# Kernel optimization log

Measured on AMD Instinct MI355X. Metric: run time of the kernel, lower is better.

The kernel has to match this reference:

```python
import jax, jax.numpy as jnp
import numpy as np

N = 2048      # num_nodes
B = 64        # batch
D_IN = 2      # input_dim per node
UNITS = 64    # hidden dim
K = 2         # max_diffusion_step
N_SUP = 2     # dual_random_walk -> two supports
M = N_SUP * K + 1           # num_matrices = 5
IN_SIZE = D_IN + UNITS      # 66
E = 65536                   # nnz per support


def setup_inputs() -> dict:
    key = jax.random.key(0)
    ks = jax.random.split(key, 10)
    inputs = jax.random.normal(ks[0], (B, N * D_IN), jnp.float32)
    state = jax.random.normal(ks[1], (B, N * UNITS), jnp.float32)
    edges1 = jax.random.randint(ks[2], (2, E), 0, N)
    vals1 = jax.random.uniform(ks[3], (E,), jnp.float32) / 32.0  # ~row-stochastic scale
    edges2 = jax.random.randint(ks[4], (2, E), 0, N)
    vals2 = jax.random.uniform(ks[5], (E,), jnp.float32) / 32.0
    W_gate = jax.random.normal(ks[6], (IN_SIZE * M, 2 * UNITS), jnp.float32) * 0.08
    b_gate = jnp.ones((2 * UNITS,), jnp.float32)  # bias_start=1.0 for gate
    W_cand = jax.random.normal(ks[7], (IN_SIZE * M, UNITS), jnp.float32) * 0.08
    b_cand = jnp.zeros((UNITS,), jnp.float32)
    return dict(inputs=inputs, state=state, edges1=edges1, vals1=vals1,
                edges2=edges2, vals2=vals2, W_gate=W_gate, b_gate=b_gate,
                W_cand=W_cand, b_cand=b_cand)


def _spmm(rows, cols, vals, x):
    # sparse [N,N] @ dense [N,F] via gather + segment_sum
    return jax.ops.segment_sum(x[cols] * vals[:, None], rows, num_segments=N)


def _dconv(inp, st, supports, W, b, out_dim):
    # inputs/state -> [B, N, F] concat, F = IN_SIZE
    x = jnp.concatenate([inp.reshape(B, N, -1), st.reshape(B, N, -1)], axis=2)
    f = x.shape[2]
    x0 = x.transpose(1, 2, 0).reshape(N, f * B)  # [N, F*B]
    xs = [x0]
    for (rows, cols, vals) in supports:
        x1 = _spmm(rows, cols, vals, x0)
        xs.append(x1)
        xk_1, xk_2 = x1, x0
        for _ in range(2, K + 1):  # Chebyshev recursion: x_k = 2 S x_{k-1} - x_{k-2}
            xk = 2.0 * _spmm(rows, cols, vals, xk_1) - xk_2
            xs.append(xk)
            xk_1, xk_2 = xk, xk_1
    xcat = jnp.stack(xs, 0).reshape(M, N, f, B)
    xcat = xcat.transpose(3, 1, 2, 0).reshape(B * N, f * M)  # [B*N, F*M]
    out = xcat @ W + b
    return out.reshape(B, N * out_dim)


def reference(inputs, state, edges1, vals1, edges2, vals2, W_gate, b_gate, W_cand, b_cand):
    supports = [(edges1[0], edges1[1], vals1), (edges2[0], edges2[1], vals2)]
    value = jax.nn.sigmoid(_dconv(inputs, state, supports, W_gate, b_gate, 2 * UNITS))
    value = value.reshape(B, N, 2 * UNITS)
    r = value[:, :, :UNITS].reshape(B, N * UNITS)
    u = value[:, :, UNITS:].reshape(B, N * UNITS)
    c = jnp.tanh(_dconv(inputs, r * state, supports, W_cand, b_cand, UNITS))
    new_state = u * state + (1.0 - u) * c
    return new_state
```

## Files before the change

### kernel.cpp

```cpp
#include <hip/hip_runtime.h>
#include <stdint.h>

#define NN 2048
#define EE 65536
#define APITCH 360
#define XSN ((size_t)NN*4096)
#define XIN ((size_t)NN*128)

typedef unsigned short u16;
typedef __bf16 bf16x8 __attribute__((ext_vector_type(8)));
typedef float f32x4 __attribute__((ext_vector_type(4)));
typedef float f32x2 __attribute__((ext_vector_type(2)));

__device__ __forceinline__ float bf2f(u16 h){ return __uint_as_float(((unsigned)h)<<16); }
__device__ __forceinline__ u16 f2bf(float f){
  unsigned u = __float_as_uint(f);
  u += 0x7fffu + ((u>>16)&1u);
  return (u16)(u>>16);
}
__device__ __forceinline__ float loadf(const void* p, size_t i, int bfflag){
  return bfflag ? bf2f(((const u16*)p)[i]) : ((const float*)p)[i];
}
__device__ __forceinline__ f32x2 up2(unsigned u){
  f32x2 r; r.x = __uint_as_float(u<<16); r.y = __uint_as_float(u & 0xffff0000u); return r;
}
__device__ __forceinline__ unsigned pk2(f32x2 t){
  return (unsigned)f2bf(t.x) | ((unsigned)f2bf(t.y)<<16);
}
__device__ __forceinline__ void accv(float v, uint4 d, f32x2* a){
  f32x2 vv = {v, v};
  a[0] += vv*up2(d.x); a[1] += vv*up2(d.y);
  a[2] += vv*up2(d.z); a[3] += vv*up2(d.w);
}

__global__ void probe_k(const unsigned* __restrict__ vals, int* __restrict__ flag){
  int i = threadIdx.x;
  unsigned lo = vals[i] & 0xffffu;
  unsigned long long m = __ballot(lo >= 0x2800u && lo < 0x3D80u);
  if (i==0) *flag = (__popcll(m) >= 32) ? 1 : 0;
}

__global__ void hist2_k(const int* __restrict__ e1, const int* __restrict__ e2,
                        int* __restrict__ cnt){
  int b = blockIdx.x;
  if (b < 256) atomicAdd(&cnt[e1[b*256 + threadIdx.x]], 1);
  else atomicAdd(&cnt[2048 + e2[(b-256)*256 + threadIdx.x]], 1);
}

__global__ void scan2_k(const int* __restrict__ cntA, int* __restrict__ rpA, int* __restrict__ curA){
  __shared__ int s[1024];
  const int* cnt = cntA + blockIdx.x*2048;
  int* rp  = rpA  + blockIdx.x*2049;
  int* cur = curA + blockIdx.x*2048;
  int t = threadIdx.x;
  int c0 = cnt[2*t], c1 = cnt[2*t+1];
  int ps = c0 + c1;
  s[t] = ps;
  __syncthreads();
  for (int off=1; off<1024; off<<=1){
    int v = (t>=off) ? s[t-off] : 0;
    __syncthreads();
    s[t] += v;
    __syncthreads();
  }
  int excl = s[t] - ps;
  rp[2*t] = excl;  cur[2*t] = excl;
  rp[2*t+1] = excl + c0;  cur[2*t+1] = excl + c0;
  if (t==0) rp[2048] = EE;
}

__global__ void scatter2_k(const int* __restrict__ e1, const void* __restrict__ v1,
                           const int* __restrict__ e2, const void* __restrict__ v2,
                           int* __restrict__ curA, int2* __restrict__ scvA,
                           const int* __restrict__ flag){
  int bfflag = *flag;
  int b = blockIdx.x;
  const int* rows; const int* cols; const void* vals; int* cur; int2* scv; int e;
  if (b < 256){ rows=e1; cols=e1+EE; vals=v1; cur=curA; scv=scvA; e=b*256+threadIdx.x; }
  else { rows=e2; cols=e2+EE; vals=v2; cur=curA+2048; scv=scvA+EE; e=(b-256)*256+threadIdx.x; }
  int r = rows[e];
  int p = atomicAdd(&cur[r], 1);
  int2 cv; cv.x = cols[e]; cv.y = __float_as_int(loadf(vals, e, bfflag));
  scv[p] = cv;
}

__global__ void pack2_k(const void* __restrict__ Wg, const void* __restrict__ Wc,
                        u16* __restrict__ Wfg, u16* __restrict__ Wfc,
                        const int* __restrict__ flag){
  int bfflag = *flag;
  int b = blockIdx.x;
  const void* W; u16* Wf; int O, OT, i;
  if (b < 176){ W=Wg; Wf=Wfg; O=128; OT=8; i=b*256+threadIdx.x; }
  else { W=Wc; Wf=Wfc; O=64; OT=4; i=(b-176)*256+threadIdx.x; }
  int j = i & 7, L = (i>>3)&63, tq = i>>9;
  int t = tq % OT, q = tq / OT;
  int o = t*16 + (L&15);
  int kk = q*32 + (L>>4)*8 + j;
  float v = 0.f;
  if (kk < 320){ int m = kk>>6, f = (kk&63)+2; v = loadf(W, (size_t)(f*5+m)*O + o, bfflag); }
  else if (kk < 330){ int tt = kk-320; int m = tt>>1, f = tt&1; v = loadf(W, (size_t)(f*5+m)*O + o, bfflag); }
  Wf[i] = f2bf(v);
}

__global__ void build_x0_k(const void* __restrict__ inp, const void* __restrict__ st,
                           u16* __restrict__ XSb, u16* __restrict__ XIb,
                           const int* __restrict__ flag){
  int bfflag = *flag, n = blockIdx.x, tid = threadIdx.x;
  if (bfflag){
    const uint4* sp = (const uint4*)st;
    uint4* xp = (uint4*)(XSb + (size_t)n*4096);
    #pragma unroll
    for (int it=0; it<2; ++it){
      int r = tid + it*256;
      int b = r>>3, v4 = r&7;
      xp[r] = sp[(size_t)b*(NN*8) + (size_t)n*8 + v4];
    }
    if (tid < 64){
      ((unsigned*)XIb)[n*64 + tid] = ((const unsigned*)inp)[(size_t)tid*NN + n];
    }
  } else {
    for (int i=tid; i<4096; i+=256){
      int b=i>>6, f=i&63;
      XSb[(size_t)n*4096+i] = f2bf(((const float*)st)[(size_t)b*(NN*64) + n*64 + f]);
    }
    for (int i=tid; i<128; i+=256){
      int b=i>>1, f=i&1;
      XIb[(size_t)n*128+i] = f2bf(((const float*)inp)[(size_t)b*(NN*2) + n*2 + f]);
    }
  }
}

template<int CHEB>
__global__ __launch_bounds__(64) void spmm_k(
    u16* __restrict__ XSb, u16* __restrict__ XIb,
    const int* __restrict__ rpA, const int2* __restrict__ scvA){
  int sup = blockIdx.y;
  const int* rp = rpA + sup*2049;
  const int2* scv = scvA + sup*EE;
  const int srcm = CHEB ? (sup?3:1) : 0;
  const int dstm = CHEB ? (sup?4:2) : (sup?3:1);
  int tid = threadIdx.x;
  int bx = blockIdx.x;
  if (bx < NN*8){
    int ch = bx & 7, n = bx >> 3;
    int e0 = rp[n], e1 = rp[n+1];
    const uint4* src = (const uint4*)(XSb + srcm*XSN);
    int off = ch*64 + tid;
    f32x2 a[4] = {{0.f,0.f},{0.f,0.f},{0.f,0.f},{0.f,0.f}};
    int e = e0;
    for (; e+3 < e1; e += 4){
      int2 c0=scv[e], c1=scv[e+1], c2=scv[e+2], c3=scv[e+3];
      uint4 d0 = src[((size_t)c0.x<<9) + off];
      uint4 d1 = src[((size_t)c1.x<<9) + off];
      uint4 d2 = src[((size_t)c2.x<<9) + off];
      uint4 d3 = src[((size_t)c3.x<<9) + off];
      accv(__int_as_float(c0.y), d0, a);
      accv(__int_as_float(c1.y), d1, a);
      accv(__int_as_float(c2.y), d2, a);
      accv(__int_as_float(c3.y), d3, a);
    }
    for (; e < e1; ++e){
      int2 c0 = scv[e];
      accv(__int_as_float(c0.y), src[((size_t)c0.x<<9) + off], a);
    }
    uint4* dst = (uint4*)(XSb + dstm*XSN);
    uint4 w;
    if (CHEB){
      uint4 o = ((const uint4*)XSb)[((size_t)n<<9) + off];
      f32x2 t;
      t = 2.f*a[0] - up2(o.x); w.x = pk2(t);
      t = 2.f*a[1] - up2(o.y); w.y = pk2(t);
      t = 2.f*a[2] - up2(o.z); w.z = pk2(t);
      t = 2.f*a[3] - up2(o.w); w.w = pk2(t);
    } else {
      w.x = pk2(a[0]); w.y = pk2(a[1]); w.z = pk2(a[2]); w.w = pk2(a[3]);
    }
    dst[((size_t)n<<9) + off] = w;
  } else {
    int idx = bx - NN*8;
    int n = idx*2 + (tid>>5), m = tid & 31;
    int e0 = rp[n], e1 = rp[n+1];
    const uint2* src = (const uint2*)(XIb + srcm*XIN);
    f32x2 a0 = {0.f,0.f}, a1 = {0.f,0.f};
    for (int e=e0; e<e1; ++e){
      int2 cv = scv[e];
      uint2 d = src[cv.x*32 + m];
      f32x2 vv = {__int_as_float(cv.y), __int_as_float(cv.y)};
      a0 += vv*up2(d.x); a1 += vv*up2(d.y);
    }
    uint2* dst = (uint2*)(XIb + dstm*XIN);
    if (CHEB){
      uint2 o = ((const uint2*)XIb)[n*32 + m];
      a0 = 2.f*a0 - up2(o.x); a1 = 2.f*a1 - up2(o.y);
    }
    uint2 w; w.x = pk2(a0); w.y = pk2(a1);
    dst[n*32 + m] = w;
  }
}

template<int OT, int MODE>
__global__ __launch_bounds__(256) void gemm_k(
    u16* __restrict__ XSb, const u16* __restrict__ XIb,
    const u16* __restrict__ Wf, const void* __restrict__ bias,
    const void* __restrict__ state, void* __restrict__ outp,
    const int* __restrict__ flag){
  __shared__ __align__(16) u16 A[64*APITCH];
  int tid = threadIdx.x, n = blockIdx.x;
  int bfflag = *flag;
  #pragma unroll
  for (int m=0;m<5;m++){
    const uint4* src = (const uint4*)(XSb + (size_t)m*XSN + ((size_t)n<<12));
    #pragma unroll
    for (int it=0; it<2; ++it){
      int r = tid + it*256;
      uint4 d = src[r];
      int b = r>>3, f0 = (r&7)*8;
      *(uint4*)&A[b*APITCH + m*64 + f0] = d;
    }
  }
  for (int i=tid; i<320; i+=256){
    int m = i>>6, b = i&63;
    unsigned v = ((const unsigned*)XIb)[(size_t)m*(XIN/2) + n*64 + b];
    *(unsigned*)&A[b*APITCH + 320 + 2*m] = v;
  }
  for (int i=tid; i<64*15; i+=256){
    int b = i/15, j = i - b*15;
    *(unsigned*)&A[b*APITCH + 330 + 2*j] = 0;
  }
  const int TW = OT/4;
  int lane = tid & 63, w = tid >> 6;
  int m16 = lane & 15, q4 = lane >> 4;
  const bf16x8* wp = (const bf16x8*)Wf;
  bf16x8 wfr[11][TW];
  #pragma unroll
  for (int q=0;q<11;q++){
    #pragma unroll
    for (int i=0;i<TW;i++) wfr[q][i] = wp[(q*OT + (w + 4*i))*64 + lane];
  }
  __syncthreads();
  #pragma unroll
  for (int rt4=0; rt4<4; ++rt4){
    const u16* arow = A + (rt4*16 + m16)*APITCH + q4*8;
    f32x4 acc[TW];
    #pragma unroll
    for (int i=0;i<TW;i++) acc[i] = (f32x4){0.f,0.f,0.f,0.f};
    #pragma unroll
    for (int q=0;q<11;q++){
      bf16x8 af = *((const bf16x8*)(arow + q*32));
      #pragma unroll
      for (int i=0;i<TW;i++)
        acc[i] = __builtin_amdgcn_mfma_f32_16x16x32_bf16(af, wfr[q][i], acc[i], 0, 0, 0);
    }
    #pragma unroll
    for (int i=0;i<TW;i++){
      int t = w + 4*i;
      int o = t*16 + m16;
      float bo = loadf(bias, o, bfflag);
      #pragma unroll
      for (int r=0;r<4;r++){
        int b = rt4*16 + q4*4 + r;
        float x = acc[i][r] + bo;
        if (MODE==0){
          float s = 1.f/(1.f + __expf(-x));
          if (i==0){
            float st = loadf(state, (size_t)b*(NN*64) + (size_t)n*64 + o, bfflag);
            XSb[((size_t)n<<12) + b*64 + o] = f2bf(s*st);
          } else {
            size_t idx = (size_t)b*(NN*64) + (size_t)n*64 + (o-64);
            if (bfflag) ((u16*)outp)[idx] = f2bf(s); else ((float*)outp)[idx] = s;
          }
        } else {
          float c = tanhf(x);
          size_t idx = (size_t)b*(NN*64) + (size_t)n*64 + o;
          float uu = bfflag ? bf2f(((const u16*)outp)[idx]) : ((const float*)outp)[idx];
          float st = loadf(state, idx, bfflag);
          float ns = uu*st + (1.f-uu)*c;
          if (bfflag) ((u16*)outp)[idx] = f2bf(ns); else ((float*)outp)[idx] = ns;
        }
      }
    }
  }
}

extern "C" void kernel_launch(void* const* d_in, const int* in_sizes, int n_in,
                              void* d_out, int out_size, void* d_ws, size_t ws_size,
                              hipStream_t stream) {
  const void* inputs = d_in[0];
  const void* state  = d_in[1];
  const int* edges1 = (const int*)d_in[2];
  const void* vals1  = d_in[3];
  const int* edges2 = (const int*)d_in[4];
  const void* vals2  = d_in[5];
  const void* Wg     = d_in[6];
  const void* bg     = d_in[7];
  const void* Wc     = d_in[8];
  const void* bc     = d_in[9];

  char* ws = (char*)d_ws;
  size_t off = 0;
  auto get = [&](size_t bytes)->void*{
    void* p = ws + off; off = (off + bytes + 255) & ~(size_t)255; return p;
  };
  u16* XSb = (u16*)get(5*XSN*2);
  u16* XIb = (u16*)get(5*XIN*2);
  u16* Wfg = (u16*)get(11*8*64*8*2);
  u16* Wfc = (u16*)get(11*4*64*8*2);
  int* cnt  = (int*)get(2*2048*4);
  int* rp   = (int*)get(2*2049*4);
  int* cur  = (int*)get(2*2048*4);
  int* flag = (int*)get(4);
  int2* scv = (int2*)get((size_t)2*EE*8);

  probe_k<<<1,64,0,stream>>>((const unsigned*)vals1, flag);
  hipMemsetAsync(cnt, 0, 2*2048*4, stream);
  hist2_k<<<512,256,0,stream>>>(edges1, edges2, cnt);
  scan2_k<<<2,1024,0,stream>>>(cnt, rp, cur);
  scatter2_k<<<512,256,0,stream>>>(edges1, vals1, edges2, vals2, cur, scv, flag);
  pack2_k<<<264,256,0,stream>>>(Wg, Wc, Wfg, Wfc, flag);
  build_x0_k<<<NN,256,0,stream>>>(inputs, state, XSb, XIb, flag);

  dim3 sg(NN*8 + NN/2, 2);
  spmm_k<0><<<sg,64,0,stream>>>(XSb, XIb, rp, scv);
  spmm_k<1><<<sg,64,0,stream>>>(XSb, XIb, rp, scv);
  gemm_k<8,0><<<NN,256,0,stream>>>(XSb, XIb, Wfg, bg, state, d_out, flag);
  spmm_k<0><<<sg,64,0,stream>>>(XSb, XIb, rp, scv);
  spmm_k<1><<<sg,64,0,stream>>>(XSb, XIb, rp, scv);
  gemm_k<4,1><<<NN,256,0,stream>>>(XSb, XIb, Wfc, bc, state, d_out, flag);
}
```

Baseline: 447.0 us.

## Widen SpMM per-thread chunk, interleave supports in 1D grid, pre-shift column offsets

The SpMM kernel now has each thread handle 32 bytes (16 bf16 values) per gathered row, using 4 chunks per node instead of 8. Both supports are interleaved in a single 1D grid so the two supports for the same node run in adjacent blocks. Column indices are pre-scaled into byte offsets during CSR scatter so the gather address is a plain add. Outputs use nontemporal stores and the Chebyshev x0 read uses nontemporal loads. This cuts index loads and address math per byte gathered, at the cost of more registers per thread and fewer waves overall.

```diff
diff --git a/kernel.cpp b/kernel.cpp
--- a/kernel.cpp
+++ b/kernel.cpp
@@ -11,6 +11,7 @@
 typedef __bf16 bf16x8 __attribute__((ext_vector_type(8)));
 typedef float f32x4 __attribute__((ext_vector_type(4)));
 typedef float f32x2 __attribute__((ext_vector_type(2)));
+typedef unsigned u32x4 __attribute__((ext_vector_type(4)));
 
 __device__ __forceinline__ float bf2f(u16 h){ return __uint_as_float(((unsigned)h)<<16); }
 __device__ __forceinline__ u16 f2bf(float f){
@@ -27,7 +28,7 @@
 __device__ __forceinline__ unsigned pk2(f32x2 t){
   return (unsigned)f2bf(t.x) | ((unsigned)f2bf(t.y)<<16);
 }
-__device__ __forceinline__ void accv(float v, uint4 d, f32x2* a){
+__device__ __forceinline__ void accv(float v, u32x4 d, f32x2* a){
   f32x2 vv = {v, v};
   a[0] += vv*up2(d.x); a[1] += vv*up2(d.y);
   a[2] += vv*up2(d.z); a[3] += vv*up2(d.w);
@@ -80,7 +81,7 @@
   else { rows=e2; cols=e2+EE; vals=v2; cur=curA+2048; scv=scvA+EE; e=(b-256)*256+threadIdx.x; }
   int r = rows[e];
   int p = atomicAdd(&cur[r], 1);
-  int2 cv; cv.x = cols[e]; cv.y = __float_as_int(loadf(vals, e, bfflag));
+  int2 cv; cv.x = cols[e] << 13; cv.y = __float_as_int(loadf(vals, e, bfflag));
   scv[p] = cv;
 }
 
@@ -134,67 +135,85 @@
 __global__ __launch_bounds__(64) void spmm_k(
     u16* __restrict__ XSb, u16* __restrict__ XIb,
     const int* __restrict__ rpA, const int2* __restrict__ scvA){
-  int sup = blockIdx.y;
-  const int* rp = rpA + sup*2049;
-  const int2* scv = scvA + sup*EE;
-  const int srcm = CHEB ? (sup?3:1) : 0;
-  const int dstm = CHEB ? (sup?4:2) : (sup?3:1);
   int tid = threadIdx.x;
   int bx = blockIdx.x;
   if (bx < NN*8){
-    int ch = bx & 7, n = bx >> 3;
+    int ch = bx & 3, sup = (bx>>2)&1, n = bx >> 3;
+    const int* rp = rpA + sup*2049;
+    const int2* scv = scvA + sup*EE;
+    const int srcm = CHEB ? (sup?3:1) : 0;
+    const int dstm = CHEB ? (sup?4:2) : (sup?3:1);
     int e0 = rp[n], e1 = rp[n+1];
-    const uint4* src = (const uint4*)(XSb + srcm*XSN);
-    int off = ch*64 + tid;
-    f32x2 a[4] = {{0.f,0.f},{0.f,0.f},{0.f,0.f},{0.f,0.f}};
+    unsigned offB = (unsigned)ch*2048 + (unsigned)tid*32;
+    const char* srcp = (const char*)(XSb + (size_t)srcm*XSN) + offB;
+    f32x2 a[8] = {{0.f,0.f},{0.f,0.f},{0.f,0.f},{0.f,0.f},
+                  {0.f,0.f},{0.f,0.f},{0.f,0.f},{0.f,0.f}};
     int e = e0;
-    for (; e+3 < e1; e += 4){
-      int2 c0=scv[e], c1=scv[e+1], c2=scv[e+2], c3=scv[e+3];
-      uint4 d0 = src[((size_t)c0.x<<9) + off];
-      uint4 d1 = src[((size_t)c1.x<<9) + off];
-      uint4 d2 = src[((size_t)c2.x<<9) + off];
-      uint4 d3 = src[((size_t)c3.x<<9) + off];
-      accv(__int_as_float(c0.y), d0, a);
-      accv(__int_as_float(c1.y), d1, a);
-      accv(__int_as_float(c2.y), d2, a);
-      accv(__int_as_float(c3.y), d3, a);
-    }
-    for (; e < e1; ++e){
+    for (; e+1 < e1; e += 2){
+      int2 c0 = scv[e], c1 = scv[e+1];
+      const char* p0 = srcp + (unsigned)c0.x;
+      const char* p1 = srcp + (unsigned)c1.x;
+      u32x4 d00 = *(const u32x4*)p0;
+      u32x4 d01 = *(const u32x4*)(p0+16);
+      u32x4 d10 = *(const u32x4*)p1;
+      u32x4 d11 = *(const u32x4*)(p1+16);
+      float v0 = __int_as_float(c0.y), v1 = __int_as_float(c1.y);
+      accv(v0, d00, a); accv(v0, d01, a+4);
+      accv(v1, d10, a); accv(v1, d11, a+4);
+    }
+    if (e < e1){
       int2 c0 = scv[e];
-      accv(__int_as_float(c0.y), src[((size_t)c0.x<<9) + off], a);
-    }
-    uint4* dst = (uint4*)(XSb + dstm*XSN);
-    uint4 w;
+      const char* p0 = srcp + (unsigned)c0.x;
+      u32x4 d00 = *(const u32x4*)p0;
+      u32x4 d01 = *(const u32x4*)(p0+16);
+      float v0 = __int_as_float(c0.y);
+      accv(v0, d00, a); accv(v0, d01, a+4);
+    }
+    unsigned doff = ((unsigned)n << 13) + offB;
+    char* dstp = (char*)(XSb + (size_t)dstm*XSN) + doff;
+    u32x4 w0, w1;
     if (CHEB){
-      uint4 o = ((const uint4*)XSb)[((size_t)n<<9) + off];
+      u32x4 o0 = __builtin_nontemporal_load((const u32x4*)((const char*)XSb + doff));
+      u32x4 o1 = __builtin_nontemporal_load((const u32x4*)((const char*)XSb + doff + 16));
       f32x2 t;
-      t = 2.f*a[0] - up2(o.x); w.x = pk2(t);
-      t = 2.f*a[1] - up2(o.y); w.y = pk2(t);
-      t = 2.f*a[2] - up2(o.z); w.z = pk2(t);
-      t = 2.f*a[3] - up2(o.w); w.w = pk2(t);
+      t = 2.f*a[0] - up2(o0.x); w0.x = pk2(t);
+      t = 2.f*a[1] - up2(o0.y); w0.y = pk2(t);
+      t = 2.f*a[2] - up2(o0.z); w0.z = pk2(t);
+      t = 2.f*a[3] - up2(o0.w); w0.w = pk2(t);
+      t = 2.f*a[4] - up2(o1.x); w1.x = pk2(t);
+      t = 2.f*a[5] - up2(o1.y); w1.y = pk2(t);
+      t = 2.f*a[6] - up2(o1.z); w1.z = pk2(t);
+      t = 2.f*a[7] - up2(o1.w); w1.w = pk2(t);
     } else {
-      w.x = pk2(a[0]); w.y = pk2(a[1]); w.z = pk2(a[2]); w.w = pk2(a[3]);
-    }
-    dst[((size_t)n<<9) + off] = w;
+      w0.x = pk2(a[0]); w0.y = pk2(a[1]); w0.z = pk2(a[2]); w0.w = pk2(a[3]);
+      w1.x = pk2(a[4]); w1.y = pk2(a[5]); w1.z = pk2(a[6]); w1.w = pk2(a[7]);
+    }
+    __builtin_nontemporal_store(w0, (u32x4*)dstp);
+    __builtin_nontemporal_store(w1, (u32x4*)(dstp+16));
   } else {
     int idx = bx - NN*8;
-    int n = idx*2 + (tid>>5), m = tid & 31;
+    int sup = idx & 1;
+    const int* rp = rpA + sup*2049;
+    const int2* scv = scvA + sup*EE;
+    const int srcm = CHEB ? (sup?3:1) : 0;
+    const int dstm = CHEB ? (sup?4:2) : (sup?3:1);
+    int n = (idx>>1)*2 + (tid>>5), m = tid & 31;
     int e0 = rp[n], e1 = rp[n+1];
-    const uint2* src = (const uint2*)(XIb + srcm*XIN);
+    const char* srcp = (const char*)(XIb + (size_t)srcm*XIN) + m*8;
     f32x2 a0 = {0.f,0.f}, a1 = {0.f,0.f};
     for (int e=e0; e<e1; ++e){
       int2 cv = scv[e];
-      uint2 d = src[cv.x*32 + m];
+      uint2 d = *(const uint2*)(srcp + ((unsigned)cv.x >> 5));
       f32x2 vv = {__int_as_float(cv.y), __int_as_float(cv.y)};
       a0 += vv*up2(d.x); a1 += vv*up2(d.y);
     }
-    uint2* dst = (uint2*)(XIb + dstm*XIN);
+    unsigned doff = (unsigned)n*256 + m*8;
     if (CHEB){
-      uint2 o = ((const uint2*)XIb)[n*32 + m];
+      uint2 o = *(const uint2*)((const char*)XIb + doff);
       a0 = 2.f*a0 - up2(o.x); a1 = 2.f*a1 - up2(o.y);
     }
-    uint2 w; w.x = pk2(a0); w.y = pk2(a1);
-    dst[n*32 + m] = w;
+    uint2 wv; wv.x = pk2(a0); wv.y = pk2(a1);
+    *(uint2*)((char*)(XIb + (size_t)dstm*XIN) + doff) = wv;
   }
 }
 
@@ -319,11 +338,11 @@
   pack2_k<<<264,256,0,stream>>>(Wg, Wc, Wfg, Wfc, flag);
   build_x0_k<<<NN,256,0,stream>>>(inputs, state, XSb, XIb, flag);
 
-  dim3 sg(NN*8 + NN/2, 2);
-  spmm_k<0><<<sg,64,0,stream>>>(XSb, XIb, rp, scv);
-  spmm_k<1><<<sg,64,0,stream>>>(XSb, XIb, rp, scv);
+  const int SG = NN*8 + NN;
+  spmm_k<0><<<SG,64,0,stream>>>(XSb, XIb, rp, scv);
+  spmm_k<1><<<SG,64,0,stream>>>(XSb, XIb, rp, scv);
   gemm_k<8,0><<<NN,256,0,stream>>>(XSb, XIb, Wfg, bg, state, d_out, flag);
-  spmm_k<0><<<sg,64,0,stream>>>(XSb, XIb, rp, scv);
-  spmm_k<1><<<sg,64,0,stream>>>(XSb, XIb, rp, scv);
+  spmm_k<0><<<SG,64,0,stream>>>(XSb, XIb, rp, scv);
+  spmm_k<1><<<SG,64,0,stream>>>(XSb, XIb, rp, scv);
   gemm_k<4,1><<<NN,256,0,stream>>>(XSb, XIb, Wfc, bc, state, d_out, flag);
 }
```

Result: slower. 482.8 us (+8.0%).
